# Kernel optimization log

Hardware: AMD Instinct MI355X
Metric: run time of the kernel (lower is better)

## Reference

```python
import jax, jax.numpy as jnp
import numpy as np

N = 60000      # total nodes (disjoint batch)
E = 240000     # total edges
F_IN = 10      # node feature dim
S = 3          # edge feature dim
C = 16         # nNodes (channel width)
G = 512        # number of graphs in batch


def setup_inputs() -> dict:
    key = jax.random.key(0)
    ks = jax.random.split(key, 24)
    sc = 0.05
    inp = {
        "x": jax.random.normal(ks[0], (N, F_IN), jnp.float32),
        "a_vals": jax.random.uniform(ks[1], (E,), jnp.float32),
        "e": jax.random.normal(ks[2], (E, S), jnp.float32),
        "edge_index": jax.random.randint(ks[3], (2, E), 0, N, jnp.int32),
        "seg": jnp.sort(jax.random.randint(ks[4], (N,), 0, G, jnp.int32)),
        # GCNConv 1/2
        "W_gcn1": jax.random.normal(ks[5], (F_IN, C), jnp.float32) * sc,
        "b_gcn1": jnp.zeros((C,), jnp.float32),
        "W_gcn2": jax.random.normal(ks[6], (C, 2 * C), jnp.float32) * sc,
        "b_gcn2": jnp.zeros((2 * C,), jnp.float32),
        # ECCConv 1 (edge kernel net: Dense(S -> F_IN*C), root kernel, bias)
        "We1": jax.random.normal(ks[7], (S, F_IN * C), jnp.float32) * sc,
        "be1": jnp.zeros((F_IN * C,), jnp.float32),
        "root1": jax.random.normal(ks[8], (F_IN, C), jnp.float32) * sc,
        "bias1": jnp.zeros((C,), jnp.float32),
        # ECCConv 2 (Dense(S -> C*2C))
        "We2": jax.random.normal(ks[9], (S, C * 2 * C), jnp.float32) * sc,
        "be2": jnp.zeros((C * 2 * C,), jnp.float32),
        "root2": jax.random.normal(ks[10], (C, 2 * C), jnp.float32) * sc,
        "bias2": jnp.zeros((2 * C,), jnp.float32),
        # MLP head: concat(2C + 2C) -> C -> C//2 -> 1
        "Wd1": jax.random.normal(ks[11], (4 * C, C), jnp.float32) * sc,
        "bd1": jnp.zeros((C,), jnp.float32),
        "Wd2": jax.random.normal(ks[12], (C, C // 2), jnp.float32) * sc,
        "bd2": jnp.zeros((C // 2,), jnp.float32),
        "Wo": jax.random.normal(ks[13], (C // 2, 1), jnp.float32) * sc,
        "bo": jnp.zeros((1,), jnp.float32),
    }
    return inp


def _spmm(rows, cols, vals, y):
    # sparse A @ y : out[i] += vals * y[j]
    return jax.ops.segment_sum(vals[:, None] * y[cols], rows, num_segments=N)


def _gcn(x, rows, cols, vals, W, b):
    return jax.nn.relu(_spmm(rows, cols, vals, x @ W) + b)


def _ecc(x, rows, cols, e, We, be, root, bias, f_in, f_out):
    # per-edge kernel matrix from edge features
    kern = (e @ We + be).reshape(-1, f_in, f_out)        # [E, Fin, Fout]
    msgs = jnp.einsum('ef,efo->eo', x[cols], kern)       # [E, Fout]
    agg = jax.ops.segment_sum(msgs, rows, num_segments=N)
    return jax.nn.relu(agg + x @ root + bias)


def reference(x, a_vals, e, edge_index, seg,
              W_gcn1, b_gcn1, W_gcn2, b_gcn2,
              We1, be1, root1, bias1,
              We2, be2, root2, bias2,
              Wd1, bd1, Wd2, bd2, Wo, bo):
    rows, cols = edge_index[0], edge_index[1]
    # GCN branch
    g1 = _gcn(x, rows, cols, a_vals, W_gcn1, b_gcn1)      # [N, C]
    g2 = _gcn(g1, rows, cols, a_vals, W_gcn2, b_gcn2)     # [N, 2C]
    # ECC branch
    c1 = _ecc(x, rows, cols, e, We1, be1, root1, bias1, F_IN, C)       # [N, C]
    c2 = _ecc(c1, rows, cols, e, We2, be2, root2, bias2, C, 2 * C)     # [N, 2C]
    # global sum pool per graph
    p1 = jax.ops.segment_sum(g2, seg, num_segments=G)     # [G, 2C]
    p2 = jax.ops.segment_sum(c2, seg, num_segments=G)     # [G, 2C]
    h = jnp.concatenate([p1, p2], axis=-1)                # [G, 4C]
    h = jax.nn.relu(h @ Wd1 + bd1)
    h = jax.nn.relu(h @ Wd2 + bd2)
    # dropout rate 0.0 -> identity (inference)
    return jax.nn.sigmoid(h @ Wo + bo)                    # [G, 1]
```

## Files before the change

kernel.cpp:

```cpp
#include <hip/hip_runtime.h>
#include <math.h>

#define N_NODES 60000
#define N_EDGES 240000
#define F_INQ 10
#define G_DIM 512
#define NB_SCAN ((N_NODES + 255) / 256)
#define NB_EDGE ((N_EDGES + 255) / 256)
#define NB_TILE ((N_NODES + 63) / 64)
#define PQ1_STRIDE 56

__global__ __launch_bounds__(256) void k_deg(
    const int* __restrict__ ei, int* __restrict__ rs)
{
    int e = blockIdx.x * 256 + threadIdx.x;
    if (e < N_EDGES) atomicAdd(&rs[ei[e]], 1);
}

__global__ __launch_bounds__(256) void k_scan_a(
    int* __restrict__ rs, int* __restrict__ bsum)
{
    __shared__ int s[256];
    int i = blockIdx.x * 256 + threadIdx.x;
    int v = (i < N_NODES) ? rs[i] : 0;
    s[threadIdx.x] = v;
    __syncthreads();
    for (int off = 1; off < 256; off <<= 1) {
        int t = (threadIdx.x >= off) ? s[threadIdx.x - off] : 0;
        __syncthreads();
        s[threadIdx.x] += t;
        __syncthreads();
    }
    if (i < N_NODES) rs[i] = s[threadIdx.x] - v;
    if (threadIdx.x == 255) bsum[blockIdx.x] = s[255];
}

__global__ __launch_bounds__(256) void k_scan_b(
    int* __restrict__ bsum,
    const float* __restrict__ Wg1, const float* __restrict__ bg1,
    const float* __restrict__ We1, const float* __restrict__ be1,
    const float* __restrict__ root1, const float* __restrict__ bias1,
    const float* __restrict__ Wg2, const float* __restrict__ bg2,
    const float* __restrict__ We2, const float* __restrict__ be2,
    const float* __restrict__ root2, const float* __restrict__ bias2,
    float* __restrict__ Wt1, float* __restrict__ Wt2)
{
    __shared__ int s[256];
    int v = (threadIdx.x < NB_SCAN) ? bsum[threadIdx.x] : 0;
    s[threadIdx.x] = v;
    __syncthreads();
    for (int off = 1; off < 256; off <<= 1) {
        int t = (threadIdx.x >= off) ? s[threadIdx.x - off] : 0;
        __syncthreads();
        s[threadIdx.x] += t;
        __syncthreads();
    }
    if (threadIdx.x < NB_SCAN) bsum[threadIdx.x] = s[threadIdx.x] - v;

    for (int i = threadIdx.x; i < 16 * 11; i += 256) {
        int o = i / 11, f = i - o * 11;
        Wt1[o * 64 + f] = (f < 10) ? Wg1[f * 16 + o] : bg1[o];
    }
    for (int i = threadIdx.x; i < 16 * 51; i += 256) {
        int o = i / 51, f = i - o * 51;
        float w;
        if      (f < 10) w = be1[f * 16 + o];
        else if (f < 20) w = We1[(f - 10) * 16 + o];
        else if (f < 30) w = We1[160 + (f - 20) * 16 + o];
        else if (f < 40) w = We1[320 + (f - 30) * 16 + o];
        else if (f < 50) w = root1[(f - 40) * 16 + o];
        else             w = bias1[o];
        Wt1[(16 + o) * 64 + f] = w;
    }
    for (int i = threadIdx.x; i < 32 * 17; i += 256) {
        int o = i / 17, f = i - o * 17;
        Wt2[o * 96 + f] = (f < 16) ? Wg2[f * 32 + o] : bg2[o];
    }
    for (int i = threadIdx.x; i < 32 * 81; i += 256) {
        int o = i / 81, f = i - o * 81;
        float w;
        if      (f < 16) w = be2[f * 32 + o];
        else if (f < 32) w = We2[(f - 16) * 32 + o];
        else if (f < 48) w = We2[512 + (f - 32) * 32 + o];
        else if (f < 64) w = We2[1024 + (f - 48) * 32 + o];
        else if (f < 80) w = root2[(f - 64) * 32 + o];
        else             w = bias2[o];
        Wt2[(32 + o) * 96 + f] = w;
    }
}

__global__ __launch_bounds__(256) void k_fill(
    const int* __restrict__ ei, const float* __restrict__ a_vals,
    const float* __restrict__ efeat,
    int* __restrict__ rs, const int* __restrict__ bsum,
    int* __restrict__ ecol, float4* __restrict__ edata)
{
    int e = blockIdx.x * 256 + threadIdx.x;
    if (e >= N_EDGES) return;
    int row = ei[e];
    int slot = atomicAdd(&rs[row], 1) + bsum[row >> 8];
    ecol[slot] = ei[N_EDGES + e];
    edata[slot] = make_float4(a_vals[e], efeat[e * 3], efeat[e * 3 + 1], efeat[e * 3 + 2]);
}

__global__ __launch_bounds__(256) void k_edge1(
    const float* __restrict__ x,
    const int* __restrict__ rs, const int* __restrict__ bsum,
    const int* __restrict__ ecol, const float4* __restrict__ edata,
    float* __restrict__ PQ1)
{
    int idx = blockIdx.x * 256 + threadIdx.x;
    int node = idx >> 4, f = idx & 15;
    if (f >= F_INQ) return;
    int end = rs[node] + bsum[node >> 8];
    int start = (node == 0) ? 0 : (rs[node - 1] + bsum[(node - 1) >> 8]);
    float p0 = 0.f, p1 = 0.f, p2 = 0.f, p3 = 0.f, q = 0.f;
    int k = start;
    for (; k + 2 <= end; k += 2) {
        int c0 = ecol[k], c1 = ecol[k + 1];
        float4 e0 = edata[k], e1 = edata[k + 1];
        float x0 = x[c0 * F_INQ + f];
        float x1 = x[c1 * F_INQ + f];
        p0 += x0;        p0 += x1;
        p1 += e0.y * x0; p1 += e1.y * x1;
        p2 += e0.z * x0; p2 += e1.z * x1;
        p3 += e0.w * x0; p3 += e1.w * x1;
        q  += e0.x * x0; q  += e1.x * x1;
    }
    if (k < end) {
        int c0 = ecol[k];
        float4 e0 = edata[k];
        float x0 = x[c0 * F_INQ + f];
        p0 += x0;
        p1 += e0.y * x0;
        p2 += e0.z * x0;
        p3 += e0.w * x0;
        q  += e0.x * x0;
    }
    float* P = PQ1 + (size_t)node * PQ1_STRIDE;
    P[f]      = p0;
    P[10 + f] = p1;
    P[20 + f] = p2;
    P[30 + f] = p3;
    P[40 + f] = q;
}

__global__ __launch_bounds__(256) void k_tf1(
    const float* __restrict__ PQ1,
    const float* __restrict__ x,
    const float* __restrict__ Wt1,
    float* __restrict__ g1c1)
{
    __shared__ float val[64][65];
    int tile = blockIdx.x;
    int lane = threadIdx.x & 63;
    int wv = __builtin_amdgcn_readfirstlane(threadIdx.x >> 6);
    int node = tile * 64 + lane;
    int nclamp = node < N_NODES ? node : N_NODES - 1;

    float pr[52];
    const float4* P4 = (const float4*)(PQ1 + (size_t)nclamp * PQ1_STRIDE);
#pragma unroll
    for (int i = 0; i < 13; ++i) {
        float4 t = P4[i];
        pr[i * 4] = t.x; pr[i * 4 + 1] = t.y; pr[i * 4 + 2] = t.z; pr[i * 4 + 3] = t.w;
    }
    float xs[10];
    const float2* X2 = (const float2*)(x + (size_t)nclamp * F_INQ);
#pragma unroll
    for (int i = 0; i < 5; ++i) {
        float2 t = X2[i];
        xs[i * 2] = t.x; xs[i * 2 + 1] = t.y;
    }

#pragma unroll
    for (int j = 0; j < 4; ++j) {
        const float* wr = Wt1 + (wv * 4 + j) * 64;
        float a = wr[10];
#pragma unroll
        for (int f = 0; f < 10; ++f) a = fmaf(wr[f], pr[40 + f], a);
        val[lane][wv * 4 + j] = a > 0.f ? a : 0.f;
    }
#pragma unroll
    for (int j = 0; j < 4; ++j) {
        const float* wr = Wt1 + (16 + wv * 4 + j) * 64;
        float a = wr[50];
#pragma unroll
        for (int f = 0; f < 40; ++f) a = fmaf(wr[f], pr[f], a);
#pragma unroll
        for (int f = 0; f < 10; ++f) a = fmaf(wr[40 + f], xs[f], a);
        val[lane][16 + wv * 4 + j] = a > 0.f ? a : 0.f;
    }
    __syncthreads();

    float4* G4 = (float4*)(g1c1 + (size_t)tile * 64 * 32);
#pragma unroll
    for (int k = 0; k < 2; ++k) {
        int fi4 = k * 256 + threadIdx.x;
        int n = fi4 >> 3, o4 = (fi4 & 7) * 4;
        if (tile * 64 + n < N_NODES)
            G4[fi4] = make_float4(val[n][o4], val[n][o4 + 1], val[n][o4 + 2], val[n][o4 + 3]);
    }
}

__global__ __launch_bounds__(256) void k_edge2(
    const float* __restrict__ g1c1,
    const int* __restrict__ rs, const int* __restrict__ bsum,
    const int* __restrict__ ecol, const float4* __restrict__ edata,
    float* __restrict__ PQ2)
{
    int idx = blockIdx.x * 256 + threadIdx.x;
    int node = idx >> 4, f = idx & 15;
    int end = rs[node] + bsum[node >> 8];
    int start = (node == 0) ? 0 : (rs[node - 1] + bsum[(node - 1) >> 8]);
    float p0 = 0.f, p1 = 0.f, p2 = 0.f, p3 = 0.f, q = 0.f;
    int k = start;
    for (; k + 2 <= end; k += 2) {
        int c0 = ecol[k], c1 = ecol[k + 1];
        float4 e0 = edata[k], e1 = edata[k + 1];
        float g0 = g1c1[c0 * 32 + f],      g1v = g1c1[c1 * 32 + f];
        float v0 = g1c1[c0 * 32 + 16 + f], v1 = g1c1[c1 * 32 + 16 + f];
        p0 += v0;        p0 += v1;
        p1 += e0.y * v0; p1 += e1.y * v1;
        p2 += e0.z * v0; p2 += e1.z * v1;
        p3 += e0.w * v0; p3 += e1.w * v1;
        q  += e0.x * g0; q  += e1.x * g1v;
    }
    if (k < end) {
        int c0 = ecol[k];
        float4 e0 = edata[k];
        float g0 = g1c1[c0 * 32 + f];
        float v0 = g1c1[c0 * 32 + 16 + f];
        p0 += v0;
        p1 += e0.y * v0;
        p2 += e0.z * v0;
        p3 += e0.w * v0;
        q  += e0.x * g0;
    }
    float* P = PQ2 + (size_t)node * 80;
    P[f]      = p0;
    P[16 + f] = p1;
    P[32 + f] = p2;
    P[48 + f] = p3;
    P[64 + f] = q;
}

__global__ __launch_bounds__(256) void k_tf2pool(
    const float* __restrict__ PQ2,
    const float* __restrict__ g1c1,
    const int* __restrict__ seg,
    const float* __restrict__ Wt2,
    float* __restrict__ pool)
{
    __shared__ float val[64][65];
    __shared__ int sseg[64];
    int tile = blockIdx.x;
    int lane = threadIdx.x & 63;
    int wv = __builtin_amdgcn_readfirstlane(threadIdx.x >> 6);
    int node = tile * 64 + lane;
    int nclamp = node < N_NODES ? node : N_NODES - 1;

    if (threadIdx.x < 64) {
        int nd = tile * 64 + threadIdx.x;
        sseg[threadIdx.x] = (nd < N_NODES) ? seg[nd] : -1;
    }

    float pr[80];
    const float4* P4 = (const float4*)(PQ2 + (size_t)nclamp * 80);
#pragma unroll
    for (int i = 0; i < 20; ++i) {
        float4 t = P4[i];
        pr[i * 4] = t.x; pr[i * 4 + 1] = t.y; pr[i * 4 + 2] = t.z; pr[i * 4 + 3] = t.w;
    }
    float cs[16];
    const float4* C4 = (const float4*)(g1c1 + (size_t)nclamp * 32 + 16);
#pragma unroll
    for (int i = 0; i < 4; ++i) {
        float4 t = C4[i];
        cs[i * 4] = t.x; cs[i * 4 + 1] = t.y; cs[i * 4 + 2] = t.z; cs[i * 4 + 3] = t.w;
    }

#pragma unroll
    for (int j = 0; j < 8; ++j) {
        const float* wr = Wt2 + (wv * 8 + j) * 96;
        float a = wr[16];
#pragma unroll
        for (int f = 0; f < 16; ++f) a = fmaf(wr[f], pr[64 + f], a);
        val[lane][wv * 8 + j] = a > 0.f ? a : 0.f;
    }
#pragma unroll
    for (int j = 0; j < 8; ++j) {
        const float* wr = Wt2 + (32 + wv * 8 + j) * 96;
        float a = wr[80];
#pragma unroll
        for (int f = 0; f < 64; ++f) a = fmaf(wr[f], pr[f], a);
#pragma unroll
        for (int f = 0; f < 16; ++f) a = fmaf(wr[64 + f], cs[f], a);
        val[lane][32 + wv * 8 + j] = a > 0.f ? a : 0.f;
    }
    __syncthreads();

    int c = threadIdx.x & 63, q = threadIdx.x >> 6;
    int base = q * 16;
    float acc = 0.f;
    int curg = -1;
    for (int n = 0; n < 16; ++n) {
        int nd = tile * 64 + base + n;
        if (nd >= N_NODES) break;
        int gsg = sseg[base + n];
        if (gsg != curg) {
            if (curg >= 0) atomicAdd(&pool[curg * 64 + c], acc);
            acc = 0.f;
            curg = gsg;
        }
        acc += val[base + n][c];
    }
    if (curg >= 0) atomicAdd(&pool[curg * 64 + c], acc);
}

__global__ __launch_bounds__(256) void k_head(
    const float* __restrict__ pool,
    const float* __restrict__ Wd1, const float* __restrict__ bd1,
    const float* __restrict__ Wd2, const float* __restrict__ bd2,
    const float* __restrict__ Wo,  const float* __restrict__ bo,
    float* __restrict__ out)
{
    __shared__ float pl[4][64];
    __shared__ float h1s[4][16];
    __shared__ float h2s[4][8];
    int q = threadIdx.x >> 6, t = threadIdx.x & 63;
    int g = blockIdx.x * 4 + q;
    pl[q][t] = pool[g * 64 + t];
    __syncthreads();
    if (t < 16) {
        float a = bd1[t];
        for (int k = 0; k < 64; ++k) a += pl[q][k] * Wd1[k * 16 + t];
        h1s[q][t] = a > 0.f ? a : 0.f;
    }
    __syncthreads();
    if (t < 8) {
        float a = bd2[t];
        for (int k = 0; k < 16; ++k) a += h1s[q][k] * Wd2[k * 8 + t];
        h2s[q][t] = a > 0.f ? a : 0.f;
    }
    __syncthreads();
    if (t == 0) {
        float a = bo[0];
        for (int k = 0; k < 8; ++k) a += h2s[q][k] * Wo[k];
        out[g] = 1.f / (1.f + expf(-a));
    }
}

extern "C" void kernel_launch(void* const* d_in, const int* in_sizes, int n_in,
                              void* d_out, int out_size, void* d_ws, size_t ws_size,
                              hipStream_t stream)
{
    const float* x      = (const float*)d_in[0];
    const float* a_vals = (const float*)d_in[1];
    const float* efeat  = (const float*)d_in[2];
    const int*   ei     = (const int*)d_in[3];
    const int*   seg    = (const int*)d_in[4];
    const float* Wg1    = (const float*)d_in[5];
    const float* bg1    = (const float*)d_in[6];
    const float* Wg2    = (const float*)d_in[7];
    const float* bg2    = (const float*)d_in[8];
    const float* We1    = (const float*)d_in[9];
    const float* be1    = (const float*)d_in[10];
    const float* root1  = (const float*)d_in[11];
    const float* bias1  = (const float*)d_in[12];
    const float* We2    = (const float*)d_in[13];
    const float* be2    = (const float*)d_in[14];
    const float* root2  = (const float*)d_in[15];
    const float* bias2  = (const float*)d_in[16];
    const float* Wd1    = (const float*)d_in[17];
    const float* bd1    = (const float*)d_in[18];
    const float* Wd2    = (const float*)d_in[19];
    const float* bd2    = (const float*)d_in[20];
    const float* Wo     = (const float*)d_in[21];
    const float* bo     = (const float*)d_in[22];

    float4* edata = (float4*)d_ws;
    float*  PQ1  = (float*)(edata + N_EDGES);
    float*  g1c1 = PQ1 + (size_t)N_NODES * PQ1_STRIDE;
    float*  PQ2  = g1c1 + (size_t)N_NODES * 32;
    float*  Wt1  = PQ2 + (size_t)N_NODES * 80;
    float*  Wt2  = Wt1 + 32 * 64;
    int*    rs   = (int*)(Wt2 + 64 * 96);
    float*  pool = (float*)(rs + N_NODES);
    int*    bsum = (int*)(pool + (size_t)G_DIM * 64);
    int*    ecol = bsum + 256;
    float*  out  = (float*)d_out;

    hipMemsetAsync(rs, 0, sizeof(int) * (N_NODES + G_DIM * 64), stream);

    k_deg    <<<NB_EDGE, 256, 0, stream>>>(ei, rs);
    k_scan_a <<<NB_SCAN, 256, 0, stream>>>(rs, bsum);
    k_scan_b <<<1, 256, 0, stream>>>(bsum, Wg1, bg1, We1, be1, root1, bias1,
                                     Wg2, bg2, We2, be2, root2, bias2, Wt1, Wt2);
    k_fill   <<<NB_EDGE, 256, 0, stream>>>(ei, a_vals, efeat, rs, bsum, ecol, edata);

    k_edge1<<<N_NODES * 16 / 256, 256, 0, stream>>>(x, rs, bsum, ecol, edata, PQ1);
    k_tf1  <<<NB_TILE, 256, 0, stream>>>(PQ1, x, Wt1, g1c1);

    k_edge2<<<N_NODES * 16 / 256, 256, 0, stream>>>(g1c1, rs, bsum, ecol, edata, PQ2);
    k_tf2pool<<<NB_TILE, 256, 0, stream>>>(PQ2, g1c1, seg, Wt2, pool);

    k_head<<<G_DIM / 4, 256, 0, stream>>>(pool, Wd1, bd1, Wd2, bd2, Wo, bo, out);
}
```

Measured before the change: 194.4 us.

## Record edge slots in degree pass, build rowptr, interleave layer-1 outputs for float2 gathers

The degree-count kernel now stores each edge's atomic slot, so the fill pass computes CSR positions without a second round of atomics, and it also writes an explicit rowptr array. The edge-1 kernel launches exactly N*10 threads instead of 16 lanes per node with 6 idle. Layer-1 outputs are stored interleaved (GCN, ECC pairs), so edge-2 reads one float2 per neighbour instead of two scalar loads. The cost is extra workspace for eslot and rowptr, plus a strided unpack of the interleaved features in the pooling kernel.

```diff
diff --git a/kernel.cpp b/kernel.cpp
--- a/kernel.cpp
+++ b/kernel.cpp
@@ -8,13 +8,14 @@
 #define NB_SCAN ((N_NODES + 255) / 256)
 #define NB_EDGE ((N_EDGES + 255) / 256)
 #define NB_TILE ((N_NODES + 63) / 64)
+#define NB_E1  ((N_NODES * F_INQ + 255) / 256)
 #define PQ1_STRIDE 56
 
 __global__ __launch_bounds__(256) void k_deg(
-    const int* __restrict__ ei, int* __restrict__ rs)
+    const int* __restrict__ ei, int* __restrict__ rs, int* __restrict__ eslot)
 {
     int e = blockIdx.x * 256 + threadIdx.x;
-    if (e < N_EDGES) atomicAdd(&rs[ei[e]], 1);
+    if (e < N_EDGES) eslot[e] = atomicAdd(&rs[ei[e]], 1);
 }
 
 __global__ __launch_bounds__(256) void k_scan_a(
@@ -91,29 +92,33 @@
 
 __global__ __launch_bounds__(256) void k_fill(
     const int* __restrict__ ei, const float* __restrict__ a_vals,
-    const float* __restrict__ efeat,
-    int* __restrict__ rs, const int* __restrict__ bsum,
-    int* __restrict__ ecol, float4* __restrict__ edata)
+    const float* __restrict__ efeat, const int* __restrict__ eslot,
+    const int* __restrict__ rs, const int* __restrict__ bsum,
+    int* __restrict__ ecol, float4* __restrict__ edata,
+    int* __restrict__ rowptr)
 {
     int e = blockIdx.x * 256 + threadIdx.x;
+    if (e <= N_NODES) {
+        rowptr[e] = (e == N_NODES) ? N_EDGES : rs[e] + bsum[e >> 8];
+    }
     if (e >= N_EDGES) return;
     int row = ei[e];
-    int slot = atomicAdd(&rs[row], 1) + bsum[row >> 8];
+    int slot = rs[row] + bsum[row >> 8] + eslot[e];
     ecol[slot] = ei[N_EDGES + e];
     edata[slot] = make_float4(a_vals[e], efeat[e * 3], efeat[e * 3 + 1], efeat[e * 3 + 2]);
 }
 
 __global__ __launch_bounds__(256) void k_edge1(
     const float* __restrict__ x,
-    const int* __restrict__ rs, const int* __restrict__ bsum,
+    const int* __restrict__ rowptr,
     const int* __restrict__ ecol, const float4* __restrict__ edata,
     float* __restrict__ PQ1)
 {
     int idx = blockIdx.x * 256 + threadIdx.x;
-    int node = idx >> 4, f = idx & 15;
-    if (f >= F_INQ) return;
-    int end = rs[node] + bsum[node >> 8];
-    int start = (node == 0) ? 0 : (rs[node - 1] + bsum[(node - 1) >> 8]);
+    if (idx >= N_NODES * F_INQ) return;
+    int node = idx / F_INQ;
+    int f = idx - node * F_INQ;
+    int start = rowptr[node], end = rowptr[node + 1];
     float p0 = 0.f, p1 = 0.f, p2 = 0.f, p3 = 0.f, q = 0.f;
     int k = start;
     for (; k + 2 <= end; k += 2) {
@@ -149,9 +154,9 @@
     const float* __restrict__ PQ1,
     const float* __restrict__ x,
     const float* __restrict__ Wt1,
-    float* __restrict__ g1c1)
-{
-    __shared__ float val[64][65];
+    float* __restrict__ gc)
+{
+    __shared__ float val[64][33];
     int tile = blockIdx.x;
     int lane = threadIdx.x & 63;
     int wv = __builtin_amdgcn_readfirstlane(threadIdx.x >> 6);
@@ -179,7 +184,7 @@
         float a = wr[10];
 #pragma unroll
         for (int f = 0; f < 10; ++f) a = fmaf(wr[f], pr[40 + f], a);
-        val[lane][wv * 4 + j] = a > 0.f ? a : 0.f;
+        val[lane][(wv * 4 + j) * 2] = a > 0.f ? a : 0.f;
     }
 #pragma unroll
     for (int j = 0; j < 4; ++j) {
@@ -189,11 +194,11 @@
         for (int f = 0; f < 40; ++f) a = fmaf(wr[f], pr[f], a);
 #pragma unroll
         for (int f = 0; f < 10; ++f) a = fmaf(wr[40 + f], xs[f], a);
-        val[lane][16 + wv * 4 + j] = a > 0.f ? a : 0.f;
-    }
-    __syncthreads();
-
-    float4* G4 = (float4*)(g1c1 + (size_t)tile * 64 * 32);
+        val[lane][(wv * 4 + j) * 2 + 1] = a > 0.f ? a : 0.f;
+    }
+    __syncthreads();
+
+    float4* G4 = (float4*)(gc + (size_t)tile * 64 * 32);
 #pragma unroll
     for (int k = 0; k < 2; ++k) {
         int fi4 = k * 256 + threadIdx.x;
@@ -204,38 +209,37 @@
 }
 
 __global__ __launch_bounds__(256) void k_edge2(
-    const float* __restrict__ g1c1,
-    const int* __restrict__ rs, const int* __restrict__ bsum,
+    const float* __restrict__ gc,
+    const int* __restrict__ rowptr,
     const int* __restrict__ ecol, const float4* __restrict__ edata,
     float* __restrict__ PQ2)
 {
     int idx = blockIdx.x * 256 + threadIdx.x;
     int node = idx >> 4, f = idx & 15;
-    int end = rs[node] + bsum[node >> 8];
-    int start = (node == 0) ? 0 : (rs[node - 1] + bsum[(node - 1) >> 8]);
+    int start = rowptr[node], end = rowptr[node + 1];
+    const float2* GC2 = (const float2*)gc;
     float p0 = 0.f, p1 = 0.f, p2 = 0.f, p3 = 0.f, q = 0.f;
     int k = start;
     for (; k + 2 <= end; k += 2) {
         int c0 = ecol[k], c1 = ecol[k + 1];
         float4 e0 = edata[k], e1 = edata[k + 1];
-        float g0 = g1c1[c0 * 32 + f],      g1v = g1c1[c1 * 32 + f];
-        float v0 = g1c1[c0 * 32 + 16 + f], v1 = g1c1[c1 * 32 + 16 + f];
-        p0 += v0;        p0 += v1;
-        p1 += e0.y * v0; p1 += e1.y * v1;
-        p2 += e0.z * v0; p2 += e1.z * v1;
-        p3 += e0.w * v0; p3 += e1.w * v1;
-        q  += e0.x * g0; q  += e1.x * g1v;
+        float2 t0 = GC2[c0 * 16 + f];
+        float2 t1 = GC2[c1 * 16 + f];
+        p0 += t0.y;        p0 += t1.y;
+        p1 += e0.y * t0.y; p1 += e1.y * t1.y;
+        p2 += e0.z * t0.y; p2 += e1.z * t1.y;
+        p3 += e0.w * t0.y; p3 += e1.w * t1.y;
+        q  += e0.x * t0.x; q  += e1.x * t1.x;
     }
     if (k < end) {
         int c0 = ecol[k];
         float4 e0 = edata[k];
-        float g0 = g1c1[c0 * 32 + f];
-        float v0 = g1c1[c0 * 32 + 16 + f];
-        p0 += v0;
-        p1 += e0.y * v0;
-        p2 += e0.z * v0;
-        p3 += e0.w * v0;
-        q  += e0.x * g0;
+        float2 t0 = GC2[c0 * 16 + f];
+        p0 += t0.y;
+        p1 += e0.y * t0.y;
+        p2 += e0.z * t0.y;
+        p3 += e0.w * t0.y;
+        q  += e0.x * t0.x;
     }
     float* P = PQ2 + (size_t)node * 80;
     P[f]      = p0;
@@ -247,7 +251,7 @@
 
 __global__ __launch_bounds__(256) void k_tf2pool(
     const float* __restrict__ PQ2,
-    const float* __restrict__ g1c1,
+    const float* __restrict__ gc,
     const int* __restrict__ seg,
     const float* __restrict__ Wt2,
     float* __restrict__ pool)
@@ -273,11 +277,11 @@
         pr[i * 4] = t.x; pr[i * 4 + 1] = t.y; pr[i * 4 + 2] = t.z; pr[i * 4 + 3] = t.w;
     }
     float cs[16];
-    const float4* C4 = (const float4*)(g1c1 + (size_t)nclamp * 32 + 16);
-#pragma unroll
-    for (int i = 0; i < 4; ++i) {
+    const float4* C4 = (const float4*)(gc + (size_t)nclamp * 32);
+#pragma unroll
+    for (int i = 0; i < 8; ++i) {
         float4 t = C4[i];
-        cs[i * 4] = t.x; cs[i * 4 + 1] = t.y; cs[i * 4 + 2] = t.z; cs[i * 4 + 3] = t.w;
+        cs[i * 2] = t.y; cs[i * 2 + 1] = t.w;
     }
 
 #pragma unroll
@@ -381,29 +385,32 @@
 
     float4* edata = (float4*)d_ws;
     float*  PQ1  = (float*)(edata + N_EDGES);
-    float*  g1c1 = PQ1 + (size_t)N_NODES * PQ1_STRIDE;
-    float*  PQ2  = g1c1 + (size_t)N_NODES * 32;
+    float*  gc   = PQ1 + (size_t)N_NODES * PQ1_STRIDE;
+    float*  PQ2  = gc + (size_t)N_NODES * 32;
     float*  Wt1  = PQ2 + (size_t)N_NODES * 80;
     float*  Wt2  = Wt1 + 32 * 64;
     int*    rs   = (int*)(Wt2 + 64 * 96);
     float*  pool = (float*)(rs + N_NODES);
     int*    bsum = (int*)(pool + (size_t)G_DIM * 64);
     int*    ecol = bsum + 256;
+    int*    eslot = ecol + N_EDGES;
+    int*    rowptr = eslot + N_EDGES;
     float*  out  = (float*)d_out;
 
     hipMemsetAsync(rs, 0, sizeof(int) * (N_NODES + G_DIM * 64), stream);
 
-    k_deg    <<<NB_EDGE, 256, 0, stream>>>(ei, rs);
+    k_deg    <<<NB_EDGE, 256, 0, stream>>>(ei, rs, eslot);
     k_scan_a <<<NB_SCAN, 256, 0, stream>>>(rs, bsum);
     k_scan_b <<<1, 256, 0, stream>>>(bsum, Wg1, bg1, We1, be1, root1, bias1,
                                      Wg2, bg2, We2, be2, root2, bias2, Wt1, Wt2);
-    k_fill   <<<NB_EDGE, 256, 0, stream>>>(ei, a_vals, efeat, rs, bsum, ecol, edata);
-
-    k_edge1<<<N_NODES * 16 / 256, 256, 0, stream>>>(x, rs, bsum, ecol, edata, PQ1);
-    k_tf1  <<<NB_TILE, 256, 0, stream>>>(PQ1, x, Wt1, g1c1);
-
-    k_edge2<<<N_NODES * 16 / 256, 256, 0, stream>>>(g1c1, rs, bsum, ecol, edata, PQ2);
-    k_tf2pool<<<NB_TILE, 256, 0, stream>>>(PQ2, g1c1, seg, Wt2, pool);
+    k_fill   <<<NB_EDGE, 256, 0, stream>>>(ei, a_vals, efeat, eslot, rs, bsum,
+                                           ecol, edata, rowptr);
+
+    k_edge1<<<NB_E1, 256, 0, stream>>>(x, rowptr, ecol, edata, PQ1);
+    k_tf1  <<<NB_TILE, 256, 0, stream>>>(PQ1, x, Wt1, gc);
+
+    k_edge2<<<N_NODES * 16 / 256, 256, 0, stream>>>(gc, rowptr, ecol, edata, PQ2);
+    k_tf2pool<<<NB_TILE, 256, 0, stream>>>(PQ2, gc, seg, Wt2, pool);
 
     k_head<<<G_DIM / 4, 256, 0, stream>>>(pool, Wd1, bd1, Wd2, bd2, Wo, bo, out);
 }
```

New measurement: 190.1 us. 2.2% less time.
